# Optimization experiments

Hardware: AMD Instinct MI355X
Metric: run time of the kernel (lower is better)

## Reference

```python
import jax, jax.numpy as jnp
import numpy as np

N = 100000        # n_nodes (entities)
B = 1024          # batch of users
S = 32            # edge_threshold (sampled edges per node)
M = 64            # adj_matrix neighbors per node
D_IN = 64         # in_channel[0]
HID = 32          # out_channel[0] == in_channel[1]
D_OUT = 64        # out_channel[1]
K_STEP = 2
NUM_SAMPLE = 32
ITEM_LO, ITEM_HI = 0, 39999
SLOPE = 0.01      # leaky_relu default negative slope


def setup_inputs() -> dict:
    key = jax.random.key(0)
    ks = jax.random.split(key, 12)
    sc = lambda *sh: 1.0 / np.sqrt(sh[-1])
    return {
        "entity_embedding": jax.random.normal(ks[0], (N, D_IN), jnp.float32) * 0.1,
        "W1l": jax.random.normal(ks[1], (HID, D_IN), jnp.float32) * sc(HID, D_IN),
        "W1r": jax.random.normal(ks[2], (HID, D_IN), jnp.float32) * sc(HID, D_IN),
        "b1": jnp.zeros((HID,), jnp.float32),
        "W2l": jax.random.normal(ks[3], (D_OUT, HID), jnp.float32) * sc(D_OUT, HID),
        "W2r": jax.random.normal(ks[4], (D_OUT, HID), jnp.float32) * sc(D_OUT, HID),
        "b2": jnp.zeros((D_OUT,), jnp.float32),
        "disc_emb": jax.random.normal(ks[5], (N, D_OUT), jnp.float32) * 0.1,
        "users": jax.random.randint(ks[6], (B,), 0, ITEM_HI + 1, jnp.int32),
        "pos": jax.random.randint(ks[7], (B,), 0, ITEM_HI + 1, jnp.int32),
        "adj_matrix": jax.random.randint(ks[8], (N, M), 0, N, jnp.int32),
        "edge_matrix": jax.random.randint(ks[9], (N, S), 0, N, jnp.int32),
    }


def _leaky(x):
    return jnp.where(x >= 0, x, SLOPE * x)


def _sage(x, src, dst, Wl, Wr, b):
    # PyG SAGEConv: lin_l(mean_{j->i} x_j) + lin_r(x_i)
    sums = jax.ops.segment_sum(x[src], dst, num_segments=N)
    cnt = jax.ops.segment_sum(jnp.ones(src.shape, x.dtype), dst, num_segments=N)
    mean = sums / jnp.maximum(cnt, 1.0)[:, None]
    return mean @ Wl.T + b + x @ Wr.T


def _gcn(x, src, dst, W1l, W1r, b1, W2l, W2r, b2):
    h = _leaky(_sage(x, src, dst, W1l, W1r, b1))   # dropout = identity (eval)
    h = _sage(h, src, dst, W2l, W2r, b2)
    nrm = jnp.sqrt(jnp.sum(h * h, axis=1, keepdims=True))
    return h / jnp.maximum(nrm, 1e-12)             # F.normalize


def _kg_step(gcn, pos_idx, users, adj, explore_flag, step):
    u_e = gcn[users]                               # [B, d]
    pos_e = gcn[pos_idx]                           # [B, d]
    one_hop = adj[pos_idx] if explore_flag == 1 else adj[users]   # [B, M]
    i_e = gcn[one_hop]                             # [B, M, d]
    p = jnp.einsum('bmd,bd->bm', _leaky(pos_e[:, None, :] * i_e), u_e)
    logits = jax.nn.softmax(p, axis=1)
    if step == 1:
        nid = jnp.argmax(logits, axis=1)[:, None]
    else:
        _, nid = jax.lax.top_k(logits, NUM_SAMPLE)
    cand = jnp.take_along_axis(one_hop, nid, axis=1)
    prob = jnp.log(jnp.take_along_axis(logits, nid, axis=1))
    if step == 1:
        return cand[:, 0], prob[:, 0]
    return cand, prob


def _filter_entity(cand, key):
    rnd = jax.random.randint(key, cand.shape, ITEM_LO, ITEM_HI + 1, dtype=cand.dtype)
    bad = (cand > ITEM_HI) | (cand < ITEM_LO)
    return jnp.where(bad, rnd, cand)


def _prune_step(disc_emb, users, pos2, negs, logits):
    # stand-in for discriminator.item_rank (no_grad in original)
    u = jax.lax.stop_gradient(disc_emb[users])
    ranking = jnp.einsum('bd,bjd->bj', u,
                         jax.lax.stop_gradient(disc_emb[pos2] - disc_emb[negs]))
    idx = jnp.argmin(ranking, axis=1)[:, None]
    good_neg = jnp.take_along_axis(negs, idx, axis=1)[:, 0]
    good_logits = jnp.take_along_axis(logits, idx, axis=1)[:, 0]
    return good_neg, good_logits


def reference(entity_embedding, W1l, W1r, b1, W2l, W2r, b2, disc_emb,
              users, pos, adj_matrix, edge_matrix):
    src = jnp.repeat(jnp.arange(N, dtype=jnp.int32), S)   # build_edge node_index
    dst = edge_matrix.reshape(-1)
    gcn = _gcn(entity_embedding, src, dst, W1l, W1r, b1, W2l, W2r, b2)
    fkey = jax.random.key(123)
    neg_list, prob_list = [], []
    p = pos
    for k in range(K_STEP):
        one_hop, one_hop_logits = _kg_step(gcn, p, users, adj_matrix, 1, 1)
        cand, two_logits = _kg_step(gcn, one_hop, users, adj_matrix, 1, 2)
        cand = _filter_entity(cand, jax.random.fold_in(fkey, 2 * k))
        pos2, _ = _kg_step(gcn, p, users, adj_matrix, 2, 2)
        pos2 = _filter_entity(pos2, jax.random.fold_in(fkey, 2 * k + 1))
        good_neg, good_logits = _prune_step(disc_emb, users, pos2, cand, two_logits)
        good_logits = good_logits + one_hop_logits
        neg_list.append(good_neg)
        prob_list.append(good_logits)
        p = good_neg
    return jnp.stack(neg_list), jnp.stack(prob_list)
```

## Files before the change

kernel.cpp:

```cpp
#include <hip/hip_runtime.h>
#include <hip/hip_bf16.h>

#define N_NODES 100000
#define N_EDGES (N_NODES * 32)
#define BATCH   1024
#define SPAN    40000u
#define MULT    7296u
#define FILL_B  (N_EDGES / 256)
#define GEMM_B  (N_NODES / 8)

#define NB_BKT 391
#define EPB    4096
#define SBLK   782


__host__ __device__ inline void threefry2x32(unsigned k0, unsigned k1,
                                             unsigned x0, unsigned x1,
                                             unsigned* o0, unsigned* o1)
{
  unsigned ks2 = k0 ^ k1 ^ 0x1BD11BDAu;
  unsigned v0 = x0 + k0, v1 = x1 + k1;
#define RL(x,d) (((x) << (d)) | ((x) >> (32 - (d))))
#define G4(a,b,c,dd) \
  v0 += v1; v1 = RL(v1,a);  v1 ^= v0; \
  v0 += v1; v1 = RL(v1,b);  v1 ^= v0; \
  v0 += v1; v1 = RL(v1,c);  v1 ^= v0; \
  v0 += v1; v1 = RL(v1,dd); v1 ^= v0;
  G4(13,15,26,6)  v0 += k1;  v1 += ks2 + 1u;
  G4(17,29,16,24) v0 += ks2; v1 += k0 + 2u;
  G4(13,15,26,6)  v0 += k0;  v1 += k1 + 3u;
  G4(17,29,16,24) v0 += k1;  v1 += ks2 + 4u;
  G4(13,15,26,6)  v0 += ks2; v1 += k0 + 5u;
#undef G4
#undef RL
  *o0 = v0; *o1 = v1;
}


__global__ __launch_bounds__(256) void k_bucket_hist(
    const int* __restrict__ edge, int* __restrict__ bhist)
{
  __shared__ int h[NB_BKT];
  for (int i = threadIdx.x; i < NB_BKT; i += 256) h[i] = 0;
  __syncthreads();
  int base = blockIdx.x * EPB;
  int cnt = N_EDGES - base; if (cnt > EPB) cnt = EPB;
  const int4* e4 = (const int4*)(edge + base);
  int nq = cnt >> 2;
  for (int i = threadIdx.x; i < nq; i += 256) {
    int4 v = e4[i];
    atomicAdd(&h[v.x >> 8], 1); atomicAdd(&h[v.y >> 8], 1);
    atomicAdd(&h[v.z >> 8], 1); atomicAdd(&h[v.w >> 8], 1);
  }
  __syncthreads();
  for (int i = threadIdx.x; i < NB_BKT; i += 256)
    if (h[i]) atomicAdd(&bhist[i], h[i]);
}

__global__ void k_scan_buckets(const int* __restrict__ bhist,
                               int* __restrict__ bbase, int* __restrict__ bcur)
{
  __shared__ int s[512];
  int t = threadIdx.x;
  s[t] = (t < NB_BKT) ? bhist[t] : 0;
  __syncthreads();
  for (int o = 1; o < 512; o <<= 1) {
    int u = (t >= o) ? s[t - o] : 0;
    __syncthreads();
    s[t] += u;
    __syncthreads();
  }
  if (t < NB_BKT) {
    int excl = s[t] - bhist[t];
    bbase[t] = excl;
    bcur[t]  = excl;
  }
}

__global__ __launch_bounds__(256) void k_bucket_scatter(
    const int* __restrict__ edge, int* __restrict__ bcur,
    int* __restrict__ pairs)
{
  __shared__ int  h[NB_BKT];
  __shared__ int  lbase[NB_BKT];
  __shared__ int  gbase[NB_BKT];
  __shared__ int  lcur[NB_BKT];
  __shared__ int2 buf[EPB];
  int t = threadIdx.x;
  for (int i = t; i < NB_BKT; i += 256) h[i] = 0;
  __syncthreads();
  int base = blockIdx.x * EPB;
  int cnt = N_EDGES - base; if (cnt > EPB) cnt = EPB;
  const int4* e4 = (const int4*)(edge + base);
  int nq = cnt >> 2;
  for (int i = t; i < nq; i += 256) {
    int4 v = e4[i];
    atomicAdd(&h[v.x >> 8], 1); atomicAdd(&h[v.y >> 8], 1);
    atomicAdd(&h[v.z >> 8], 1); atomicAdd(&h[v.w >> 8], 1);
  }
  __syncthreads();
  if (t < 64) {
    int run = 0;
    for (int c = 0; c < NB_BKT; c += 64) {
      int idx = c + t;
      int v = (idx < NB_BKT) ? h[idx] : 0;
      int orig = v;
      for (int o = 1; o < 64; o <<= 1) {
        int u = __shfl_up(v, o);
        if (t >= o) v += u;
      }
      if (idx < NB_BKT) lbase[idx] = run + v - orig;
      run += __shfl(v, 63);
    }
  }
  __syncthreads();
  for (int i = t; i < NB_BKT; i += 256) lcur[i] = lbase[i];
  __syncthreads();
  for (int i = t; i < nq; i += 256) {
    int4 v = e4[i];
    int eid = base + (i << 2);
    int p;
    p = atomicAdd(&lcur[v.x >> 8], 1); buf[p] = make_int2(v.x, (eid + 0) >> 5);
    p = atomicAdd(&lcur[v.y >> 8], 1); buf[p] = make_int2(v.y, (eid + 1) >> 5);
    p = atomicAdd(&lcur[v.z >> 8], 1); buf[p] = make_int2(v.z, (eid + 2) >> 5);
    p = atomicAdd(&lcur[v.w >> 8], 1); buf[p] = make_int2(v.w, (eid + 3) >> 5);
  }
  __syncthreads();
  for (int i = t; i < NB_BKT; i += 256) {
    int c = lcur[i] - lbase[i];
    gbase[i] = (c > 0) ? atomicAdd(&bcur[i], c) : 0;
  }
  __syncthreads();
  for (int i = t; i < cnt; i += 256) {
    int2 pr = buf[i];
    int b = pr.x >> 8;
    pairs[gbase[b] + (i - lbase[b])] = (pr.y << 8) | (pr.x & 255);
  }
}

__global__ __launch_bounds__(256) void k_bucket_csr(
    const int* __restrict__ bbase, const int* __restrict__ bhist,
    const int* __restrict__ pairs, int* __restrict__ csr,
    int* __restrict__ rowp, int* __restrict__ deg)
{
  __shared__ int nd[256], nb[256], nc[256];
  int b = blockIdx.x, t = threadIdx.x;
  int nb0 = b << 8;
  int ebase = bbase[b];
  int ecnt  = bhist[b];
  nd[t] = 0; nc[t] = 0;
  __syncthreads();
  for (int i = t; i < ecnt; i += 256) {
    int pr = pairs[ebase + i];
    atomicAdd(&nd[pr & 255], 1);
  }
  __syncthreads();
  nb[t] = nd[t];
  __syncthreads();
  for (int o = 1; o < 256; o <<= 1) {
    int u = (t >= o) ? nb[t - o] : 0;
    __syncthreads();
    nb[t] += u;
    __syncthreads();
  }
  int excl = nb[t] - nd[t];
  int node = nb0 + t;
  if (node < N_NODES) { rowp[node] = ebase + excl; deg[node] = nd[t]; }
  __syncthreads();
  nb[t] = excl;
  __syncthreads();
  for (int i = t; i < ecnt; i += 256) {
    int pr = pairs[ebase + i];
    int l = pr & 255;
    int p = atomicAdd(&nc[l], 1);
    csr[ebase + nb[l] + p] = pr >> 8;
  }
}

__global__ __launch_bounds__(256) void k_gather_csr(
    const int* __restrict__ rowp, const int* __restrict__ deg,
    const int* __restrict__ csr, const float* __restrict__ src,
    float* __restrict__ out)
{
  int node = blockIdx.x * 8 + (threadIdx.x >> 5);
  int f = threadIdx.x & 31;
  int hb = threadIdx.x & 32;
  int sub = f >> 3;
  int q   = f & 7;
  int start = rowp[node];
  int dg = deg[node];
  const float4* src4 = (const float4*)src;
  float4 a0 = make_float4(0.f, 0.f, 0.f, 0.f);
  float4 a1 = make_float4(0.f, 0.f, 0.f, 0.f);
  for (int b0 = 0; b0 < dg; b0 += 32) {
    int idx = b0 + f;
    int e = (idx < dg) ? csr[start + idx] : -1;
#pragma unroll
    for (int j = 0; j < 8; j += 2) {
      int e0 = __shfl(e, hb + 4 * j + sub);
      int e1 = __shfl(e, hb + 4 * (j + 1) + sub);
      if (e0 >= 0) {
        float4 v = src4[(size_t)e0 * 8 + q];
        a0.x += v.x; a0.y += v.y; a0.z += v.z; a0.w += v.w;
      }
      if (e1 >= 0) {
        float4 v = src4[(size_t)e1 * 8 + q];
        a1.x += v.x; a1.y += v.y; a1.z += v.z; a1.w += v.w;
      }
    }
  }
  a0.x += a1.x; a0.y += a1.y; a0.z += a1.z; a0.w += a1.w;
  a0.x += __shfl_xor(a0.x, 8);  a0.y += __shfl_xor(a0.y, 8);
  a0.z += __shfl_xor(a0.z, 8);  a0.w += __shfl_xor(a0.w, 8);
  a0.x += __shfl_xor(a0.x, 16); a0.y += __shfl_xor(a0.y, 16);
  a0.z += __shfl_xor(a0.z, 16); a0.w += __shfl_xor(a0.w, 16);
  if (sub == 0) ((float4*)out)[(size_t)node * 8 + q] = a0;
}

__global__ __launch_bounds__(256) void k_fill_gemm(
    const int* __restrict__ edge, int* __restrict__ head, int* __restrict__ next,
    int nsub, const float* __restrict__ x, const float* __restrict__ W,
    float* __restrict__ y)
{
  __shared__ float sw[32 * 65];
  if (blockIdx.x < FILL_B) {
    int e = blockIdx.x * 256 + threadIdx.x;
    int d = edge[e];
    int sub = e & (nsub - 1);
    int old = atomicExch(head + sub * N_NODES + d, e);
    next[e] = old;
  } else {
    for (int t = threadIdx.x; t < 2048; t += 256) sw[(t >> 6) * 65 + (t & 63)] = W[t];
    __syncthreads();
    int i = (blockIdx.x - FILL_B) * 8 + (threadIdx.x >> 5);
    int f = threadIdx.x & 31;
    const float* xr = x + (size_t)i * 64;
    const float* wr = sw + f * 65;
    float acc = 0.f;
#pragma unroll
    for (int d = 0; d < 64; ++d) acc += xr[d] * wr[d];
    y[(size_t)i * 32 + f] = acc;
  }
}

template<int NSUB>
__global__ __launch_bounds__(256) void k_gather_ll(
    const int* __restrict__ head, const int* __restrict__ next,
    const float* __restrict__ src, float* __restrict__ out,
    int* __restrict__ deg_out)
{
  int node = blockIdx.x * 8 + (threadIdx.x >> 5);
  int f = threadIdx.x & 31;
  int hb = threadIdx.x & 32;
  int e = (f < NSUB) ? head[f * N_NODES + node] : -1;
  float acc = 0.f;
  int cnt = 0;
  while (true) {
    int es[NSUB];
    bool any = false;
#pragma unroll
    for (int j = 0; j < NSUB; ++j) { es[j] = __shfl(e, hb + j); any |= (es[j] != -1); }
    if (!any) break;
    int en = -1;
    if (f < NSUB && e != -1) en = next[e];
#pragma unroll
    for (int j = 0; j < NSUB; ++j)
      if (es[j] != -1) { acc += src[(size_t)(es[j] >> 5) * 32 + f]; cnt++; }
    e = en;
  }
  out[(size_t)node * 32 + f] = acc;
  if (deg_out != nullptr && f == 0) deg_out[node] = cnt;
}


__global__ __launch_bounds__(256) void k_gemm64x32(
    const float* __restrict__ x, const float* __restrict__ W, float* __restrict__ y)
{
  __shared__ float sw[32 * 65];
  for (int t = threadIdx.x; t < 2048; t += 256) sw[(t >> 6) * 65 + (t & 63)] = W[t];
  __syncthreads();
  int i = blockIdx.x * 8 + (threadIdx.x >> 5);
  int f = threadIdx.x & 31;
  const float* xr = x + (size_t)i * 64;
  const float* wr = sw + f * 65;
  float acc = 0.f;
#pragma unroll
  for (int d = 0; d < 64; ++d) acc += xr[d] * wr[d];
  y[(size_t)i * 32 + f] = acc;
}

__global__ __launch_bounds__(256) void k_scatter(
    const int* __restrict__ edge, const float* __restrict__ src,
    float* __restrict__ acc, int* __restrict__ cnt)
{
  int e = blockIdx.x * 8 + (threadIdx.x >> 5);
  int f = threadIdx.x & 31;
  int d = edge[e];
  atomicAdd(acc + (size_t)d * 32 + f, src[(size_t)(e >> 5) * 32 + f]);
  if (cnt != nullptr && f == 0) atomicAdd(cnt + d, 1);
}

__global__ __launch_bounds__(256) void k_layer1(
    const float* __restrict__ sum1, const int* __restrict__ cnt,
    const float* __restrict__ x, const float* __restrict__ W1r,
    const float* __restrict__ b1, float* __restrict__ h)
{
  __shared__ float sw[32 * 65];
  __shared__ float sb[32];
  for (int t = threadIdx.x; t < 2048; t += 256) sw[(t >> 6) * 65 + (t & 63)] = W1r[t];
  if (threadIdx.x < 32) sb[threadIdx.x] = b1[threadIdx.x];
  __syncthreads();
  int i = blockIdx.x * 8 + (threadIdx.x >> 5);
  int f = threadIdx.x & 31;
  float c = fmaxf((float)cnt[i], 1.f);
  float mean = sum1[(size_t)i * 32 + f] / c;
  const float* xr = x + (size_t)i * 64;
  const float* wr = sw + f * 65;
  float acc = 0.f;
#pragma unroll
  for (int d = 0; d < 64; ++d) acc += xr[d] * wr[d];
  float v = (mean + sb[f]) + acc;
  h[(size_t)i * 32 + f] = (v >= 0.f) ? v : 0.01f * v;
}

#define L2_BLOCKS 1250
#define L2_NPW    20
__device__ __forceinline__ float bcastf(float v, int l)
{
  return __int_as_float(__builtin_amdgcn_readlane(__float_as_int(v), l));
}

__global__ __launch_bounds__(256) void k_layer2(
    float* __restrict__ A, float* __restrict__ B, const int* __restrict__ cnt,
    const float* __restrict__ W2l, const float* __restrict__ W2r,
    const float* __restrict__ b2)
{
  int lane = threadIdx.x & 63;
  int gw = blockIdx.x * 4 + (threadIdx.x >> 6);
  float wl[32], wr[32];
#pragma unroll
  for (int f = 0; f < 32; ++f) { wl[f] = W2l[lane * 32 + f]; wr[f] = W2r[lane * 32 + f]; }
  float bb = b2[lane];
  int n0 = gw * L2_NPW;
#pragma unroll 1
  for (int i = n0; i < n0 + L2_NPW; ++i) {
    float c = fmaxf((float)cnt[i], 1.f);
    float vin;
    if (lane < 32) vin = B[(size_t)i * 32 + lane] / c;
    else           vin = A[(size_t)i * 32 + (lane - 32)];
    float acc = 0.f, acc2 = 0.f;
#pragma unroll
    for (int f = 0; f < 32; ++f) {
      acc  += bcastf(vin, f)      * wl[f];
      acc2 += bcastf(vin, 32 + f) * wr[f];
    }
    float t = (acc + bb) + acc2;
    float s = t * t;
#pragma unroll
    for (int o = 32; o > 0; o >>= 1) s += __shfl_xor(s, o);
    float g = t / fmaxf(sqrtf(s), 1e-12f);
    if (lane < 32) A[(size_t)i * 32 + lane]        = g;
    else           B[(size_t)i * 32 + (lane - 32)] = g;
  }
}


__device__ inline float kg_score(const float* __restrict__ glo,
                                 const float* __restrict__ ghi,
                                 const float* sp, const float* su, int nb)
{
  const float* rl = glo + (size_t)nb * 32;
  const float* rh = ghi + (size_t)nb * 32;
  float acc = 0.f;
#pragma unroll
  for (int d = 0; d < 32; ++d) {
    float t = sp[d] * rl[d];
    t = (t >= 0.f) ? t : 0.01f * t;
    acc += t * su[d];
  }
#pragma unroll
  for (int d = 0; d < 32; ++d) {
    float t = sp[32 + d] * rh[d];
    t = (t >= 0.f) ? t : 0.01f * t;
    acc += t * su[32 + d];
  }
  return acc;
}

__device__ inline float wave_softmax(float acc)
{
  float m = acc;
#pragma unroll
  for (int o = 32; o > 0; o >>= 1) m = fmaxf(m, __shfl_xor(m, o));
  float e = expf(acc - m);
  float Z = e;
#pragma unroll
  for (int o = 32; o > 0; o >>= 1) Z += __shfl_xor(Z, o);
  return e / Z;
}

__device__ inline void load_row(const float* glo, const float* ghi, int node,
                                int lane, float* smem)
{
  smem[lane] = (lane < 32) ? glo[(size_t)node * 32 + lane]
                           : ghi[(size_t)node * 32 + (lane - 32)];
}

__global__ __launch_bounds__(64) void k_kg_argmax(
    const float* __restrict__ glo, const float* __restrict__ ghi,
    const int* __restrict__ users, const int* __restrict__ pvec,
    const int* __restrict__ adj, int* __restrict__ sel_out,
    float* __restrict__ logit_out)
{
  int b = blockIdx.x, lane = threadIdx.x;
  int u = users[b], pb = pvec[b];
  __shared__ float su[64], sp[64];
  load_row(glo, ghi, u,  lane, su);
  load_row(glo, ghi, pb, lane, sp);
  __syncthreads();
  int nb = adj[(size_t)pb * 64 + lane];
  float sm = wave_softmax(kg_score(glo, ghi, sp, su, nb));
  float v = sm; int i = lane;
#pragma unroll
  for (int o = 32; o > 0; o >>= 1) {
    float ov = __shfl_xor(v, o); int oi = __shfl_xor(i, o);
    if (ov > v || (ov == v && oi < i)) { v = ov; i = oi; }
  }
  float smw = __shfl(sm, i);
  int sel = __shfl(nb, i);
  if (lane == 0) { sel_out[b] = sel; logit_out[b] = logf(smw); }
}

__global__ __launch_bounds__(64) void k_kg_topk2(
    const float* __restrict__ glo, const float* __restrict__ ghi,
    const int* __restrict__ users, const int* __restrict__ srcA,
    const int* __restrict__ pvecB, const int* __restrict__ adj,
    unsigned a1a, unsigned a1b, unsigned a2a, unsigned a2b,
    unsigned c1a, unsigned c1b, unsigned c2a, unsigned c2b,
    int* __restrict__ candA, float* __restrict__ logA, int* __restrict__ candB)
{
  int b = blockIdx.x & (BATCH - 1);
  int var = blockIdx.x >> 10;
  int lane = threadIdx.x;
  int u = users[b];
  int pidx = (var == 0) ? srcA[b] : pvecB[b];
  int nbr  = (var == 0) ? srcA[b] : u;
  unsigned k1a = (var == 0) ? a1a : c1a, k1b = (var == 0) ? a1b : c1b;
  unsigned k2a = (var == 0) ? a2a : c2a, k2b = (var == 0) ? a2b : c2b;
  int* cand_out = (var == 0) ? candA : candB;
  float* logit_out = (var == 0) ? logA : nullptr;

  __shared__ float su[64], sp[64];
  load_row(glo, ghi, u,    lane, su);
  load_row(glo, ghi, pidx, lane, sp);
  __syncthreads();
  int nb = adj[(size_t)nbr * 64 + lane];
  float sm = wave_softmax(kg_score(glo, ghi, sp, su, nb));
  float work = sm;
  int mysel = 0;
#pragma unroll 1
  for (int it = 0; it < 32; ++it) {
    float v = work; int i = lane;
#pragma unroll
    for (int o = 32; o > 0; o >>= 1) {
      float ov = __shfl_xor(v, o); int oi = __shfl_xor(i, o);
      if (ov > v || (ov == v && oi < i)) { v = ov; i = oi; }
    }
    if (lane == it) mysel = i;
    if (lane == i)  work = -1.0f;
  }
  float selsm = __shfl(sm, mysel);
  int   selnb = __shfl(nb, mysel);
  if (lane < 32) {
    int cand = selnb;
    if (logit_out != nullptr) logit_out[b * 32 + lane] = logf(selsm);
    unsigned j = (unsigned)(b * 32 + lane);
    unsigned h0, h1, l0, l1;
    threefry2x32(k1a, k1b, 0u, j, &h0, &h1);
    threefry2x32(k2a, k2b, 0u, j, &l0, &l1);
    unsigned hi = h0 ^ h1, lo = l0 ^ l1;
    unsigned rnd = ((hi % SPAN) * MULT + (lo % SPAN)) % SPAN;
    if (cand > 39999 || cand < 0) cand = (int)rnd;
    cand_out[b * 32 + lane] = cand;
  }
}

__global__ __launch_bounds__(64) void k_kg_prune(
    const float* __restrict__ disc, const int* __restrict__ users,
    const int* __restrict__ cand, const float* __restrict__ two_log,
    const int* __restrict__ pos2, const float* __restrict__ one_log,
    float* __restrict__ out, int k, int* __restrict__ p_next)
{
  int b = blockIdx.x, lane = threadIdx.x;
  __shared__ float su[64];
  su[lane] = disc[(size_t)users[b] * 64 + lane];
  __syncthreads();
  float r = 1e30f;
  if (lane < 32) {
    const float* dp = disc + (size_t)pos2[b * 32 + lane] * 64;
    const float* dn = disc + (size_t)cand[b * 32 + lane] * 64;
    float acc = 0.f;
#pragma unroll
    for (int d = 0; d < 64; ++d) acc += su[d] * (dp[d] - dn[d]);
    r = acc;
  }
  float v = r; int i = lane;
#pragma unroll
  for (int o = 32; o > 0; o >>= 1) {
    float ov = __shfl_xor(v, o); int oi = __shfl_xor(i, o);
    if (ov < v || (ov == v && oi < i)) { v = ov; i = oi; }
  }
  if (lane == 0) {
    int gn = cand[b * 32 + i];
    float gl = two_log[b * 32 + i] + one_log[b];
    out[k * BATCH + b]             = (float)gn;
    out[2 * BATCH + k * BATCH + b] = gl;
    p_next[b] = gn;
  }
}

extern "C" void kernel_launch(void* const* d_in, const int* in_sizes, int n_in,
                              void* d_out, int out_size, void* d_ws, size_t ws_size,
                              hipStream_t stream)
{
  const float* x    = (const float*)d_in[0];
  const float* W1l  = (const float*)d_in[1];
  const float* W1r  = (const float*)d_in[2];
  const float* b1   = (const float*)d_in[3];
  const float* W2l  = (const float*)d_in[4];
  const float* W2r  = (const float*)d_in[5];
  const float* b2   = (const float*)d_in[6];
  const float* disc = (const float*)d_in[7];
  const int*   users= (const int*)d_in[8];
  const int*   pos  = (const int*)d_in[9];
  const int*   adj  = (const int*)d_in[10];
  const int*   edge = (const int*)d_in[11];
  float* out = (float*)d_out;

  char* w = (char*)d_ws;
  const size_t NEED_CSR = 39617792;
  const size_t NEED8 = 42414080;
  const size_t NEED2 = 39710720;
  float *A, *B;
  char* bb;

  if (ws_size >= NEED_CSR) {
    int*  csr   = (int*)(w);
    int*  rowp  = (int*)(w + 12800000);
    int*  deg   = (int*)(w + 13200000);
    int*  bhist = (int*)(w + 13600000);
    int*  bbase = (int*)(w + 13604096);
    int*  bcur  = (int*)(w + 13608192);
    int*  pairs = (int*)(w + 13612288);
    A = (float*)(w + 13612288);
    B = (float*)(w + 26412288);
    bb = w + 39212288;
    hipMemsetAsync(bhist, 0, 4096, stream);
    k_bucket_hist<<<SBLK, 256, 0, stream>>>(edge, bhist);
    k_scan_buckets<<<1, 512, 0, stream>>>(bhist, bbase, bcur);
    k_bucket_scatter<<<SBLK, 256, 0, stream>>>(edge, bcur, pairs);
    k_bucket_csr<<<NB_BKT, 256, 0, stream>>>(bbase, bhist, pairs, csr, rowp, deg);
    k_gemm64x32<<<GEMM_B, 256, 0, stream>>>(x, W1l, A);
    k_gather_csr<<<N_NODES / 8, 256, 0, stream>>>(rowp, deg, csr, A, B);
    k_layer1<<<N_NODES / 8, 256, 0, stream>>>(B, deg, x, W1r, b1, A);
    k_gather_csr<<<N_NODES / 8, 256, 0, stream>>>(rowp, deg, csr, A, B);
    k_layer2<<<L2_BLOCKS, 256, 0, stream>>>(A, B, deg, W2l, W2r, b2);
  } else if (ws_size >= NEED8) {
    int* head   = (int*)(w);
    int* degbuf = (int*)(w + 3200000);
    int* next   = (int*)(w + 3604480);
    A = (float*)(w + 16404480);
    B = (float*)(w + 29204480);
    bb = w + 42004480;
    hipMemsetAsync(head, 0xFF, 3200000, stream);
    k_fill_gemm<<<FILL_B + GEMM_B, 256, 0, stream>>>(edge, head, next, 8, x, W1l, A);
    k_gather_ll<8><<<N_NODES / 8, 256, 0, stream>>>(head, next, A, B, degbuf);
    k_layer1<<<N_NODES / 8, 256, 0, stream>>>(B, degbuf, x, W1r, b1, A);
    k_gather_ll<8><<<N_NODES / 8, 256, 0, stream>>>(head, next, A, B, nullptr);
    k_layer2<<<L2_BLOCKS, 256, 0, stream>>>(A, B, degbuf, W2l, W2r, b2);
  } else if (ws_size >= NEED2) {
    int* head   = (int*)(w);
    bb = w + 800000;
    int* degbuf = (int*)(bb);
    int* next   = (int*)(w + 1310720);
    A = (float*)(w + 14110720);
    B = (float*)(w + 26910720);
    hipMemsetAsync(head, 0xFF, 800000, stream);
    k_fill_gemm<<<FILL_B + GEMM_B, 256, 0, stream>>>(edge, head, next, 2, x, W1l, A);
    k_gather_ll<2><<<N_NODES / 8, 256, 0, stream>>>(head, next, A, B, degbuf);
    k_layer1<<<N_NODES / 8, 256, 0, stream>>>(B, degbuf, x, W1r, b1, A);
    k_gather_ll<2><<<N_NODES / 8, 256, 0, stream>>>(head, next, A, B, nullptr);
    k_layer2<<<L2_BLOCKS, 256, 0, stream>>>(A, B, degbuf, W2l, W2r, b2);
  } else {
    int* cnt = (int*)w;
    A = (float*)(w + 409600);
    B = (float*)(w + 13209600);
    bb = w + 26009600;
    hipMemsetAsync(cnt, 0, 400000, stream);
    hipMemsetAsync(B, 0, 12800000, stream);
    k_gemm64x32<<<GEMM_B, 256, 0, stream>>>(x, W1l, A);
    k_scatter<<<N_EDGES / 8, 256, 0, stream>>>(edge, A, B, cnt);
    k_layer1<<<GEMM_B, 256, 0, stream>>>(B, cnt, x, W1r, b1, A);
    hipMemsetAsync(B, 0, 12800000, stream);
    k_scatter<<<N_EDGES / 8, 256, 0, stream>>>(edge, A, B, nullptr);
    k_layer2<<<L2_BLOCKS, 256, 0, stream>>>(A, B, cnt, W2l, W2r, b2);
  }

  int*   p_cur       = (int*)(bb);
  int*   one_hop_sel = (int*)(bb + 4096);
  float* one_hop_log = (float*)(bb + 8192);
  int*   cand        = (int*)(bb + 12288);
  float* two_log     = (float*)(bb + 143360);
  int*   pos2        = (int*)(bb + 274432);

  for (int k = 0; k < 2; ++k) {
    unsigned f0, f1, a1a, a1b, a2a, a2b, c1a, c1b, c2a, c2b;
    threefry2x32(0u, 123u, 0u, (unsigned)(2 * k), &f0, &f1);
    threefry2x32(f0, f1, 0u, 0u, &a1a, &a1b);
    threefry2x32(f0, f1, 0u, 1u, &a2a, &a2b);
    threefry2x32(0u, 123u, 0u, (unsigned)(2 * k + 1), &f0, &f1);
    threefry2x32(f0, f1, 0u, 0u, &c1a, &c1b);
    threefry2x32(f0, f1, 0u, 1u, &c2a, &c2b);

    const int* pvec = (k == 0) ? pos : p_cur;
    k_kg_argmax<<<BATCH, 64, 0, stream>>>(A, B, users, pvec, adj, one_hop_sel, one_hop_log);
    k_kg_topk2<<<2 * BATCH, 64, 0, stream>>>(A, B, users, one_hop_sel, pvec, adj,
                                             a1a, a1b, a2a, a2b, c1a, c1b, c2a, c2b,
                                             cand, two_log, pos2);
    k_kg_prune<<<BATCH, 64, 0, stream>>>(disc, users, cand, two_log, pos2,
                                         one_hop_log, out, k, p_cur);
  }
}
```

Baseline: 498.7 us.

## Halve CSR bucket size, register-resident GEMM weights, and rank-based top-32 selection

Bucketing for the CSR build now uses 128-node buckets (782 of them) with 2048 edges per block, which shrinks the per-block shared-memory footprint and adds parallelism. The layer-1 GEMMs keep the weight row in registers and broadcast inputs with readlane, each wave handling 20 nodes, instead of staging weights in LDS per block. The iterative 32-round argmax top-k in the KG step becomes a single pass that computes each lane's rank and writes it to slot r. The register-heavy GEMM may reduce occupancy, and the rank-based selection relies on strict tie-breaking by lane index to stay equivalent to the old ordering.

```diff
diff --git a/kernel.cpp b/kernel.cpp
--- a/kernel.cpp
+++ b/kernel.cpp
@@ -7,11 +7,10 @@
 #define SPAN    40000u
 #define MULT    7296u
 #define FILL_B  (N_EDGES / 256)
-#define GEMM_B  (N_NODES / 8)
-
-#define NB_BKT 391
-#define EPB    4096
-#define SBLK   782
+
+#define NB_BKT 782
+#define EPB    2048
+#define SBLK   ((N_EDGES + EPB - 1) / EPB)
 
 
 __host__ __device__ inline void threefry2x32(unsigned k0, unsigned k1,
@@ -36,6 +35,11 @@
   *o0 = v0; *o1 = v1;
 }
 
+__device__ __forceinline__ float bcastf(float v, int l)
+{
+  return __int_as_float(__builtin_amdgcn_readlane(__float_as_int(v), l));
+}
+
 
 __global__ __launch_bounds__(256) void k_bucket_hist(
     const int* __restrict__ edge, int* __restrict__ bhist)
@@ -49,8 +53,8 @@
   int nq = cnt >> 2;
   for (int i = threadIdx.x; i < nq; i += 256) {
     int4 v = e4[i];
-    atomicAdd(&h[v.x >> 8], 1); atomicAdd(&h[v.y >> 8], 1);
-    atomicAdd(&h[v.z >> 8], 1); atomicAdd(&h[v.w >> 8], 1);
+    atomicAdd(&h[v.x >> 7], 1); atomicAdd(&h[v.y >> 7], 1);
+    atomicAdd(&h[v.z >> 7], 1); atomicAdd(&h[v.w >> 7], 1);
   }
   __syncthreads();
   for (int i = threadIdx.x; i < NB_BKT; i += 256)
@@ -60,11 +64,11 @@
 __global__ void k_scan_buckets(const int* __restrict__ bhist,
                                int* __restrict__ bbase, int* __restrict__ bcur)
 {
-  __shared__ int s[512];
+  __shared__ int s[1024];
   int t = threadIdx.x;
   s[t] = (t < NB_BKT) ? bhist[t] : 0;
   __syncthreads();
-  for (int o = 1; o < 512; o <<= 1) {
+  for (int o = 1; o < 1024; o <<= 1) {
     int u = (t >= o) ? s[t - o] : 0;
     __syncthreads();
     s[t] += u;
@@ -95,8 +99,8 @@
   int nq = cnt >> 2;
   for (int i = t; i < nq; i += 256) {
     int4 v = e4[i];
-    atomicAdd(&h[v.x >> 8], 1); atomicAdd(&h[v.y >> 8], 1);
-    atomicAdd(&h[v.z >> 8], 1); atomicAdd(&h[v.w >> 8], 1);
+    atomicAdd(&h[v.x >> 7], 1); atomicAdd(&h[v.y >> 7], 1);
+    atomicAdd(&h[v.z >> 7], 1); atomicAdd(&h[v.w >> 7], 1);
   }
   __syncthreads();
   if (t < 64) {
@@ -120,10 +124,10 @@
     int4 v = e4[i];
     int eid = base + (i << 2);
     int p;
-    p = atomicAdd(&lcur[v.x >> 8], 1); buf[p] = make_int2(v.x, (eid + 0) >> 5);
-    p = atomicAdd(&lcur[v.y >> 8], 1); buf[p] = make_int2(v.y, (eid + 1) >> 5);
-    p = atomicAdd(&lcur[v.z >> 8], 1); buf[p] = make_int2(v.z, (eid + 2) >> 5);
-    p = atomicAdd(&lcur[v.w >> 8], 1); buf[p] = make_int2(v.w, (eid + 3) >> 5);
+    p = atomicAdd(&lcur[v.x >> 7], 1); buf[p] = make_int2(v.x, (eid + 0) >> 5);
+    p = atomicAdd(&lcur[v.y >> 7], 1); buf[p] = make_int2(v.y, (eid + 1) >> 5);
+    p = atomicAdd(&lcur[v.z >> 7], 1); buf[p] = make_int2(v.z, (eid + 2) >> 5);
+    p = atomicAdd(&lcur[v.w >> 7], 1); buf[p] = make_int2(v.w, (eid + 3) >> 5);
   }
   __syncthreads();
   for (int i = t; i < NB_BKT; i += 256) {
@@ -133,8 +137,8 @@
   __syncthreads();
   for (int i = t; i < cnt; i += 256) {
     int2 pr = buf[i];
-    int b = pr.x >> 8;
-    pairs[gbase[b] + (i - lbase[b])] = (pr.y << 8) | (pr.x & 255);
+    int b = pr.x >> 7;
+    pairs[gbase[b] + (i - lbase[b])] = (pr.y << 7) | (pr.x & 127);
   }
 }
 
@@ -143,37 +147,38 @@
     const int* __restrict__ pairs, int* __restrict__ csr,
     int* __restrict__ rowp, int* __restrict__ deg)
 {
-  __shared__ int nd[256], nb[256], nc[256];
+  __shared__ int nd[128], nb[128], nc[128];
   int b = blockIdx.x, t = threadIdx.x;
-  int nb0 = b << 8;
+  int nb0 = b << 7;
   int ebase = bbase[b];
   int ecnt  = bhist[b];
-  nd[t] = 0; nc[t] = 0;
+  if (t < 128) { nd[t] = 0; nc[t] = 0; }
   __syncthreads();
   for (int i = t; i < ecnt; i += 256) {
     int pr = pairs[ebase + i];
-    atomicAdd(&nd[pr & 255], 1);
-  }
-  __syncthreads();
-  nb[t] = nd[t];
-  __syncthreads();
-  for (int o = 1; o < 256; o <<= 1) {
-    int u = (t >= o) ? nb[t - o] : 0;
+    atomicAdd(&nd[pr & 127], 1);
+  }
+  __syncthreads();
+  if (t < 128) nb[t] = nd[t];
+  __syncthreads();
+  for (int o = 1; o < 128; o <<= 1) {
+    int u = (t >= o && t < 128) ? nb[t - o] : 0;
     __syncthreads();
-    nb[t] += u;
+    if (t < 128) nb[t] += u;
     __syncthreads();
   }
-  int excl = nb[t] - nd[t];
-  int node = nb0 + t;
-  if (node < N_NODES) { rowp[node] = ebase + excl; deg[node] = nd[t]; }
-  __syncthreads();
-  nb[t] = excl;
+  if (t < 128) {
+    int excl = nb[t] - nd[t];
+    int node = nb0 + t;
+    if (node < N_NODES) { rowp[node] = ebase + excl; deg[node] = nd[t]; }
+    nb[t] = excl;
+  }
   __syncthreads();
   for (int i = t; i < ecnt; i += 256) {
     int pr = pairs[ebase + i];
-    int l = pr & 255;
+    int l = pr & 127;
     int p = atomicAdd(&nc[l], 1);
-    csr[ebase + nb[l] + p] = pr >> 8;
+    csr[ebase + nb[l] + p] = pr >> 7;
   }
 }
 
@@ -272,21 +277,27 @@
   if (deg_out != nullptr && f == 0) deg_out[node] = cnt;
 }
 
+#define DWB 1250
+#define DNPW 20
 
 __global__ __launch_bounds__(256) void k_gemm64x32(
     const float* __restrict__ x, const float* __restrict__ W, float* __restrict__ y)
 {
-  __shared__ float sw[32 * 65];
-  for (int t = threadIdx.x; t < 2048; t += 256) sw[(t >> 6) * 65 + (t & 63)] = W[t];
-  __syncthreads();
-  int i = blockIdx.x * 8 + (threadIdx.x >> 5);
-  int f = threadIdx.x & 31;
-  const float* xr = x + (size_t)i * 64;
-  const float* wr = sw + f * 65;
-  float acc = 0.f;
-#pragma unroll
-  for (int d = 0; d < 64; ++d) acc += xr[d] * wr[d];
-  y[(size_t)i * 32 + f] = acc;
+  int lane = threadIdx.x & 63;
+  int gw = blockIdx.x * 4 + (threadIdx.x >> 6);
+  float wreg[64];
+  const float* wrow = W + (size_t)(lane & 31) * 64;
+#pragma unroll
+  for (int d = 0; d < 64; ++d) wreg[d] = wrow[d];
+  int n0 = gw * DNPW;
+#pragma unroll 1
+  for (int i = n0; i < n0 + DNPW; ++i) {
+    float vin = x[(size_t)i * 64 + lane];
+    float acc = 0.f;
+#pragma unroll
+    for (int d = 0; d < 64; ++d) acc += bcastf(vin, d) * wreg[d];
+    if (lane < 32) y[(size_t)i * 32 + lane] = acc;
+  }
 }
 
 __global__ __launch_bounds__(256) void k_scatter(
@@ -305,31 +316,31 @@
     const float* __restrict__ x, const float* __restrict__ W1r,
     const float* __restrict__ b1, float* __restrict__ h)
 {
-  __shared__ float sw[32 * 65];
-  __shared__ float sb[32];
-  for (int t = threadIdx.x; t < 2048; t += 256) sw[(t >> 6) * 65 + (t & 63)] = W1r[t];
-  if (threadIdx.x < 32) sb[threadIdx.x] = b1[threadIdx.x];
-  __syncthreads();
-  int i = blockIdx.x * 8 + (threadIdx.x >> 5);
-  int f = threadIdx.x & 31;
-  float c = fmaxf((float)cnt[i], 1.f);
-  float mean = sum1[(size_t)i * 32 + f] / c;
-  const float* xr = x + (size_t)i * 64;
-  const float* wr = sw + f * 65;
-  float acc = 0.f;
-#pragma unroll
-  for (int d = 0; d < 64; ++d) acc += xr[d] * wr[d];
-  float v = (mean + sb[f]) + acc;
-  h[(size_t)i * 32 + f] = (v >= 0.f) ? v : 0.01f * v;
+  int lane = threadIdx.x & 63;
+  int gw = blockIdx.x * 4 + (threadIdx.x >> 6);
+  float wreg[64];
+  const float* wrow = W1r + (size_t)(lane & 31) * 64;
+#pragma unroll
+  for (int d = 0; d < 64; ++d) wreg[d] = wrow[d];
+  float sb = b1[lane & 31];
+  int n0 = gw * DNPW;
+#pragma unroll 1
+  for (int i = n0; i < n0 + DNPW; ++i) {
+    float vin = x[(size_t)i * 64 + lane];
+    float acc = 0.f;
+#pragma unroll
+    for (int d = 0; d < 64; ++d) acc += bcastf(vin, d) * wreg[d];
+    if (lane < 32) {
+      float c = fmaxf((float)cnt[i], 1.f);
+      float mean = sum1[(size_t)i * 32 + lane] / c;
+      float v = (mean + sb) + acc;
+      h[(size_t)i * 32 + lane] = (v >= 0.f) ? v : 0.01f * v;
+    }
+  }
 }
 
 #define L2_BLOCKS 1250
 #define L2_NPW    20
-__device__ __forceinline__ float bcastf(float v, int l)
-{
-  return __int_as_float(__builtin_amdgcn_readlane(__float_as_int(v), l));
-}
-
 __global__ __launch_bounds__(256) void k_layer2(
     float* __restrict__ A, float* __restrict__ B, const int* __restrict__ cnt,
     const float* __restrict__ W2l, const float* __restrict__ W2r,
@@ -456,32 +467,23 @@
   __syncthreads();
   int nb = adj[(size_t)nbr * 64 + lane];
   float sm = wave_softmax(kg_score(glo, ghi, sp, su, nb));
-  float work = sm;
-  int mysel = 0;
-#pragma unroll 1
-  for (int it = 0; it < 32; ++it) {
-    float v = work; int i = lane;
-#pragma unroll
-    for (int o = 32; o > 0; o >>= 1) {
-      float ov = __shfl_xor(v, o); int oi = __shfl_xor(i, o);
-      if (ov > v || (ov == v && oi < i)) { v = ov; i = oi; }
-    }
-    if (lane == it) mysel = i;
-    if (lane == i)  work = -1.0f;
-  }
-  float selsm = __shfl(sm, mysel);
-  int   selnb = __shfl(nb, mysel);
-  if (lane < 32) {
-    int cand = selnb;
-    if (logit_out != nullptr) logit_out[b * 32 + lane] = logf(selsm);
-    unsigned j = (unsigned)(b * 32 + lane);
+  int r = 0;
+#pragma unroll
+  for (int j = 0; j < 64; ++j) {
+    float sj = bcastf(sm, j);
+    if (sj > sm || (sj == sm && j < lane)) ++r;
+  }
+  if (r < 32) {
+    int cand = nb;
+    if (logit_out != nullptr) logit_out[b * 32 + r] = logf(sm);
+    unsigned j = (unsigned)(b * 32 + r);
     unsigned h0, h1, l0, l1;
     threefry2x32(k1a, k1b, 0u, j, &h0, &h1);
     threefry2x32(k2a, k2b, 0u, j, &l0, &l1);
     unsigned hi = h0 ^ h1, lo = l0 ^ l1;
     unsigned rnd = ((hi % SPAN) * MULT + (lo % SPAN)) % SPAN;
     if (cand > 39999 || cand < 0) cand = (int)rnd;
-    cand_out[b * 32 + lane] = cand;
+    cand_out[b * 32 + r] = cand;
   }
 }
 
@@ -557,12 +559,12 @@
     bb = w + 39212288;
     hipMemsetAsync(bhist, 0, 4096, stream);
     k_bucket_hist<<<SBLK, 256, 0, stream>>>(edge, bhist);
-    k_scan_buckets<<<1, 512, 0, stream>>>(bhist, bbase, bcur);
+    k_scan_buckets<<<1, 1024, 0, stream>>>(bhist, bbase, bcur);
     k_bucket_scatter<<<SBLK, 256, 0, stream>>>(edge, bcur, pairs);
     k_bucket_csr<<<NB_BKT, 256, 0, stream>>>(bbase, bhist, pairs, csr, rowp, deg);
-    k_gemm64x32<<<GEMM_B, 256, 0, stream>>>(x, W1l, A);
+    k_gemm64x32<<<DWB, 256, 0, stream>>>(x, W1l, A);
     k_gather_csr<<<N_NODES / 8, 256, 0, stream>>>(rowp, deg, csr, A, B);
-    k_layer1<<<N_NODES / 8, 256, 0, stream>>>(B, deg, x, W1r, b1, A);
+    k_layer1<<<DWB, 256, 0, stream>>>(B, deg, x, W1r, b1, A);
     k_gather_csr<<<N_NODES / 8, 256, 0, stream>>>(rowp, deg, csr, A, B);
     k_layer2<<<L2_BLOCKS, 256, 0, stream>>>(A, B, deg, W2l, W2r, b2);
   } else if (ws_size >= NEED8) {
@@ -573,9 +575,9 @@
     B = (float*)(w + 29204480);
     bb = w + 42004480;
     hipMemsetAsync(head, 0xFF, 3200000, stream);
-    k_fill_gemm<<<FILL_B + GEMM_B, 256, 0, stream>>>(edge, head, next, 8, x, W1l, A);
+    k_fill_gemm<<<FILL_B + N_NODES / 8, 256, 0, stream>>>(edge, head, next, 8, x, W1l, A);
     k_gather_ll<8><<<N_NODES / 8, 256, 0, stream>>>(head, next, A, B, degbuf);
-    k_layer1<<<N_NODES / 8, 256, 0, stream>>>(B, degbuf, x, W1r, b1, A);
+    k_layer1<<<DWB, 256, 0, stream>>>(B, degbuf, x, W1r, b1, A);
     k_gather_ll<8><<<N_NODES / 8, 256, 0, stream>>>(head, next, A, B, nullptr);
     k_layer2<<<L2_BLOCKS, 256, 0, stream>>>(A, B, degbuf, W2l, W2r, b2);
   } else if (ws_size >= NEED2) {
@@ -586,9 +588,9 @@
     A = (float*)(w + 14110720);
     B = (float*)(w + 26910720);
     hipMemsetAsync(head, 0xFF, 800000, stream);
-    k_fill_gemm<<<FILL_B + GEMM_B, 256, 0, stream>>>(edge, head, next, 2, x, W1l, A);
+    k_fill_gemm<<<FILL_B + N_NODES / 8, 256, 0, stream>>>(edge, head, next, 2, x, W1l, A);
     k_gather_ll<2><<<N_NODES / 8, 256, 0, stream>>>(head, next, A, B, degbuf);
-    k_layer1<<<N_NODES / 8, 256, 0, stream>>>(B, degbuf, x, W1r, b1, A);
+    k_layer1<<<DWB, 256, 0, stream>>>(B, degbuf, x, W1r, b1, A);
     k_gather_ll<2><<<N_NODES / 8, 256, 0, stream>>>(head, next, A, B, nullptr);
     k_layer2<<<L2_BLOCKS, 256, 0, stream>>>(A, B, degbuf, W2l, W2r, b2);
   } else {
@@ -598,9 +600,9 @@
     bb = w + 26009600;
     hipMemsetAsync(cnt, 0, 400000, stream);
     hipMemsetAsync(B, 0, 12800000, stream);
-    k_gemm64x32<<<GEMM_B, 256, 0, stream>>>(x, W1l, A);
+    k_gemm64x32<<<DWB, 256, 0, stream>>>(x, W1l, A);
     k_scatter<<<N_EDGES / 8, 256, 0, stream>>>(edge, A, B, cnt);
-    k_layer1<<<GEMM_B, 256, 0, stream>>>(B, cnt, x, W1r, b1, A);
+    k_layer1<<<DWB, 256, 0, stream>>>(B, cnt, x, W1r, b1, A);
     hipMemsetAsync(B, 0, 12800000, stream);
     k_scatter<<<N_EDGES / 8, 256, 0, stream>>>(edge, A, B, nullptr);
     k_layer2<<<L2_BLOCKS, 256, 0, stream>>>(A, B, cnt, W2l, W2r, b2);
```

Measured after the change: 515.5 us. 1.03x slower.
